# Kernel optimization log

Measured on AMD Instinct MI355X. Metric: run time of the kernel, lower is better.

Reference implementation:

```python
import jax, jax.numpy as jnp
import numpy as np

DIM = 1024
N_HEADS = 16
DIM_FF = 4096
EPS = 1e-12


def layer_norm(x, gamma, beta):
    u = jnp.mean(x, axis=-1, keepdims=True)
    s = jnp.mean((x - u) ** 2, axis=-1, keepdims=True)
    return gamma * ((x - u) / jnp.sqrt(s + EPS)) + beta


def setup_inputs() -> dict:
    key = jax.random.key(0)
    ks = jax.random.split(key, 12)
    B, S, D, F = 2, 2048, DIM, DIM_FF
    init = lambda k, shape: (jax.random.normal(k, shape, dtype=jnp.float32) * 0.02)
    return {
        "x": jax.random.normal(ks[0], (B, S, D), dtype=jnp.float32),
        "mask": jnp.ones((B, S), dtype=jnp.int32),
        "wq": init(ks[1], (D, D)), "bq": jnp.zeros((D,), jnp.float32),
        "wk": init(ks[2], (D, D)), "bk": jnp.zeros((D,), jnp.float32),
        "wv": init(ks[3], (D, D)), "bv": jnp.zeros((D,), jnp.float32),
        "wo": init(ks[4], (D, D)), "bo": jnp.zeros((D,), jnp.float32),
        "g1": jnp.ones((D,), jnp.float32), "b1": jnp.zeros((D,), jnp.float32),
        "w1": init(ks[5], (D, F)), "bf1": jnp.zeros((F,), jnp.float32),
        "w2": init(ks[6], (F, D)), "bf2": jnp.zeros((D,), jnp.float32),
        "g2": jnp.ones((D,), jnp.float32), "b2": jnp.zeros((D,), jnp.float32),
    }


def reference(x, mask, wq, bq, wk, bk, wv, bv, wo, bo, g1, b1, w1, bf1, w2, bf2, g2, b2):
    B, S, D = x.shape
    H = N_HEADS
    W = D // H
    # QKV projections -> (B, H, S, W)
    def heads(y):
        return y.reshape(B, S, H, W).transpose(0, 2, 1, 3)
    q = heads(x @ wq + bq)
    k = heads(x @ wk + bk)
    v = heads(x @ wv + bv)
    # scaled dot-product attention with additive mask (exact module math)
    scores = jnp.einsum('bhsw,bhtw->bhst', q, k) / np.sqrt(W).astype(np.float32)
    m = mask.astype(jnp.float32)[:, None, None, :]  # (B,1,1,S)
    scores = scores - 10000.0 * (1.0 - m)
    attn = jax.nn.softmax(scores, axis=-1)
    h = jnp.einsum('bhst,bhtw->bhsw', attn, v).transpose(0, 2, 1, 3).reshape(B, S, D)
    # residual + LN1
    h = layer_norm(x + (h @ wo + bo), g1, b1)
    # position-wise FFN with exact-erf GELU, residual + LN2
    ff = jax.nn.gelu(h @ w1 + bf1, approximate=False) @ w2 + bf2
    return layer_norm(h + ff, g2, b2)
```

## Files before the change

kernel.cpp:

```cpp
#include <hip/hip_runtime.h>
#include <cstdint>
#include <cstddef>

using u16 = unsigned short;
using u32 = unsigned int;

typedef __bf16 bf16x8 __attribute__((ext_vector_type(8)));
typedef float f32x4 __attribute__((ext_vector_type(4)));

static constexpr int Bb = 2, S = 2048, D = 1024, H = 16, W = 64, F = 4096;
static constexpr int M = Bb * S;

__device__ __forceinline__ float bf2f(u16 u) {
  union { u32 i; float f; } c; c.i = ((u32)u) << 16; return c.f;
}
__device__ __forceinline__ u16 f2bf(float f) {
  union { float f; u32 i; } c; c.f = f;
  u32 i = c.i;
  u32 r = (i + 0x7fffu + ((i >> 16) & 1u)) >> 16;
  return (u16)r;
}
__device__ __forceinline__ u16 f2bf_cvt(float f) {
  __bf16 b = (__bf16)f;
  union { __bf16 b; u16 u; } c; c.b = b; return c.u;
}
__device__ __forceinline__ __bf16 u2b(u16 x) {
  union { u16 u; __bf16 b; } c; c.u = x; return c.b;
}
__device__ __forceinline__ void stv(float* p, size_t i, float v) { p[i] = v; }
__device__ __forceinline__ void stv(u16* p, size_t i, float v)   { p[i] = f2bf(v); }
__device__ __forceinline__ float ldv(const float* p, size_t i) { return p[i]; }
__device__ __forceinline__ float ldv(const u16* p, size_t i)   { return bf2f(p[i]); }

__device__ __forceinline__ void async_cp16(const u16* g, u16* l) {
  __builtin_amdgcn_global_load_lds(
      (const __attribute__((address_space(1))) void*)g,
      (__attribute__((address_space(3))) void*)l, 16, 0, 0);
}

__device__ __forceinline__ void swizzle8(int& bx, int& by) {
  int bid = blockIdx.y * gridDim.x + blockIdx.x;
  int gpr = gridDim.x >> 3;
  int grp = bid >> 6, rem = bid & 63;
  int gm = grp / gpr, gn = grp - gm * gpr;
  by = gm * 8 + (rem >> 3);
  bx = gn * 8 + (rem & 7);
}

__global__ __launch_bounds__(256) void conv_x_kernel(
    const float* __restrict__ src, u16* __restrict__ dst)
{
  int i = (blockIdx.x * 256 + threadIdx.x) * 4;
  float4 v = *(const float4*)(src + i);
  u16 r[4] = { f2bf(v.x), f2bf(v.y), f2bf(v.z), f2bf(v.w) };
  *(uint2*)(dst + i) = *(const uint2*)r;
}

__global__ __launch_bounds__(256) void transpose_w_kernel(
    const float* __restrict__ src, u16* __restrict__ dst, int K, int N)
{
  __shared__ __align__(16) u16 T[64][72];
  const int tid = threadIdx.x;
  const int n0 = blockIdx.x * 64, k0 = blockIdx.y * 64;
#pragma unroll
  for (int t = 0; t < 4; t++) {
    int idx = tid + t * 256;
    int r = idx >> 4, c4 = (idx & 15) * 4;
    float4 v = *(const float4*)(src + (size_t)(k0 + r) * N + n0 + c4);
    T[c4 + 0][r] = f2bf(v.x); T[c4 + 1][r] = f2bf(v.y);
    T[c4 + 2][r] = f2bf(v.z); T[c4 + 3][r] = f2bf(v.w);
  }
  __syncthreads();
#pragma unroll
  for (int t = 0; t < 2; t++) {
    int idx = tid + t * 256;
    int r = idx >> 3, c8 = (idx & 7) * 8;
    *(uint4*)(dst + (size_t)(n0 + r) * K + k0 + c8) = *(const uint4*)(&T[r][c8]);
  }
}

template<int EPI, typename TC>
__global__ __launch_bounds__(256) void gemm_bt(
    const u16* __restrict__ A, const u16* __restrict__ BT,
    const float* __restrict__ bias, TC* __restrict__ C,
    int N, int K, float scale)
{
  __shared__ __align__(16) u16 As[2][128 * 32];
  __shared__ __align__(16) u16 Bs[2][128 * 32];
  const int tid = threadIdx.x;
  const int wave = tid >> 6, lane = tid & 63;
  const int quad = lane >> 4, l16 = lane & 15;
  int bx, by; swizzle8(bx, by);
  const int m0 = by * 128, n0 = bx * 128;
  const int wm = (wave >> 1) * 64, wn = (wave & 1) * 64;
  const int srow = lane >> 2;
  const int skoff = (lane & 3) * 8;

  f32x4 acc[4][4] = {};

  for (int k0 = 0; k0 < K; k0 += 64) {
#pragma unroll
    for (int h = 0; h < 2; h++) {
#pragma unroll
      for (int t = 0; t < 2; t++) {
        int slot = wave * 2 + t;
        int row = slot * 16 + srow;
        const u16* ga = A  + (size_t)(m0 + row) * K + k0 + h * 32 + skoff;
        const u16* gb = BT + (size_t)(n0 + row) * K + k0 + h * 32 + skoff;
        async_cp16(ga, As[h] + slot * 512);
        async_cp16(gb, Bs[h] + slot * 512);
      }
    }
    __syncthreads();

#pragma unroll
    for (int h = 0; h < 2; h++) {
      bf16x8 af[4], bfv[4];
#pragma unroll
      for (int i = 0; i < 4; i++)
        af[i] = *(const bf16x8*)(As[h] + (wm + i * 16 + l16) * 32 + quad * 8);
#pragma unroll
      for (int j = 0; j < 4; j++)
        bfv[j] = *(const bf16x8*)(Bs[h] + (wn + j * 16 + l16) * 32 + quad * 8);
#pragma unroll
      for (int i = 0; i < 4; i++)
#pragma unroll
        for (int j = 0; j < 4; j++)
          acc[i][j] = __builtin_amdgcn_mfma_f32_16x16x32_bf16(af[i], bfv[j], acc[i][j], 0, 0, 0);
    }
    __syncthreads();
  }

#pragma unroll
  for (int i = 0; i < 4; i++) {
#pragma unroll
    for (int j = 0; j < 4; j++) {
#pragma unroll
      for (int r = 0; r < 4; r++) {
        int row = m0 + wm + i * 16 + quad * 4 + r;
        int col = n0 + wn + j * 16 + l16;
        float val = acc[i][j][r] + bias[col];
        if (EPI == 1) {
          val = 0.5f * val * (1.0f + erff(val * 0.70710678118654752f));
        }
        if (EPI == 2) {
          int sel = col >> 10, c = col & 1023;
          if (sel == 0) val *= scale;
          int bb = row >> 11, ss = row & 2047;
          int hh = c >> 6,  ww = c & 63;
          u16* dst = (u16*)C + (size_t)sel * M * D;
          dst[(((size_t)(bb * H + hh) * S) + ss) * W + ww] = f2bf(val);
        } else {
          stv(C, (size_t)row * N + col, val);
        }
      }
    }
  }
}

template<typename TC>
__global__ __launch_bounds__(256) void gemm_bt_n64(
    const u16* __restrict__ A, const u16* __restrict__ BT,
    const float* __restrict__ bias, TC* __restrict__ C,
    int N, int K)
{
  __shared__ __align__(16) u16 As[2][128 * 32];
  __shared__ __align__(16) u16 Bs[2][64 * 32];
  const int tid = threadIdx.x;
  const int wave = tid >> 6, lane = tid & 63;
  const int quad = lane >> 4, l16 = lane & 15;
  int bx, by; swizzle8(bx, by);
  const int m0 = by * 128, n0 = bx * 64;
  const int wm = (wave >> 1) * 64, wn = (wave & 1) * 32;
  const int srow = lane >> 2;
  const int skoff = (lane & 3) * 8;

  f32x4 acc[4][2] = {};

  for (int k0 = 0; k0 < K; k0 += 64) {
#pragma unroll
    for (int h = 0; h < 2; h++) {
#pragma unroll
      for (int t = 0; t < 2; t++) {
        int slot = wave * 2 + t;
        int row = slot * 16 + srow;
        async_cp16(A + (size_t)(m0 + row) * K + k0 + h * 32 + skoff, As[h] + slot * 512);
      }
      int row = wave * 16 + srow;
      async_cp16(BT + (size_t)(n0 + row) * K + k0 + h * 32 + skoff, Bs[h] + wave * 512);
    }
    __syncthreads();

#pragma unroll
    for (int h = 0; h < 2; h++) {
      bf16x8 af[4], bfv[2];
#pragma unroll
      for (int i = 0; i < 4; i++)
        af[i] = *(const bf16x8*)(As[h] + (wm + i * 16 + l16) * 32 + quad * 8);
#pragma unroll
      for (int j = 0; j < 2; j++)
        bfv[j] = *(const bf16x8*)(Bs[h] + (wn + j * 16 + l16) * 32 + quad * 8);
#pragma unroll
      for (int i = 0; i < 4; i++)
#pragma unroll
        for (int j = 0; j < 2; j++)
          acc[i][j] = __builtin_amdgcn_mfma_f32_16x16x32_bf16(af[i], bfv[j], acc[i][j], 0, 0, 0);
    }
    __syncthreads();
  }

#pragma unroll
  for (int i = 0; i < 4; i++) {
#pragma unroll
    for (int j = 0; j < 2; j++) {
#pragma unroll
      for (int r = 0; r < 4; r++) {
        int row = m0 + wm + i * 16 + quad * 4 + r;
        int col = n0 + wn + j * 16 + l16;
        stv(C, (size_t)row * N + col, acc[i][j][r] + bias[col]);
      }
    }
  }
}

__global__ __launch_bounds__(256) void transpose_v_kernel(
    const u16* __restrict__ v, u16* __restrict__ vt)
{
  __shared__ __align__(16) u16 T[64][72];
  const int bh = blockIdx.y, k0 = blockIdx.x * 64, tid = threadIdx.x;
#pragma unroll
  for (int it = 0; it < 2; it++) {
    int vv = tid + it * 256;
    int key = vv >> 3, w0 = (vv & 7) * 8;
    union { uint4 q; u16 e[8]; } u;
    u.q = *(const uint4*)(v + ((size_t)bh * S + k0 + key) * W + w0);
#pragma unroll
    for (int j = 0; j < 8; j++) T[w0 + j][key] = u.e[j];
  }
  __syncthreads();
#pragma unroll
  for (int it = 0; it < 2; it++) {
    int vv = tid + it * 256;
    int w = vv >> 3, koff = (vv & 7) * 8;
    *(uint4*)(vt + ((size_t)bh * W + w) * S + k0 + koff) = *(const uint4*)(&T[w][koff]);
  }
}

__global__ __launch_bounds__(256) void fattn_kernel(
    const u16* __restrict__ q, const u16* __restrict__ k,
    const u16* __restrict__ vt, const int* __restrict__ mask,
    u16* __restrict__ o_parts, float* __restrict__ l_parts)
{
  __shared__ __align__(16) u16 QP[2][64][32];
  __shared__ __align__(16) u16 Kl[2][64][32];
  __shared__ __align__(16) u16 Vl[2][64][32];
  __shared__ float msk[64];

  const int tid = threadIdx.x, wave = tid >> 6, lane = tid & 63;
  const int quad = lane >> 4, l16 = lane & 15;
  const int bh = blockIdx.y, b = bh >> 4, h = bh & 15;
  const int q0 = blockIdx.x * 64;
  const int half = blockIdx.z;
  const int kbase = half * (S / 2);
  const int w16 = wave * 16;
  const int sr  = tid >> 3;
  const int sg  = tid & 7;
  const int sp  = sg >> 2;
  const int sc0 = sg * 8;
  const int ssw = (((sg & 3) ^ ((sr >> 1) & 3)) << 3);
  const int rq = ((quad ^ ((l16 >> 1) & 3)) << 3);

  *(uint4*)(&QP[sp][sr     ][ssw]) = *(const uint4*)(q + ((size_t)bh * S + q0 + sr     ) * W + sc0);
  *(uint4*)(&QP[sp][sr + 32][ssw]) = *(const uint4*)(q + ((size_t)bh * S + q0 + sr + 32) * W + sc0);
  __syncthreads();
  bf16x8 aq[2];
#pragma unroll
  for (int kc = 0; kc < 2; kc++)
    aq[kc] = *(const bf16x8*)(&QP[kc][w16 + l16][rq]);

  bf16x8 ones;
  {
    u16 ov = (l16 == 0) ? (u16)0x3F80 : (u16)0;
#pragma unroll
    for (int j = 0; j < 8; j++) ones[j] = u2b(ov);
  }

  f32x4 o_acc[4] = {};
  f32x4 l_acc = {};

  uint4 kr0, kr1, vr0, vr1;
  int mv = 0;
  kr0 = *(const uint4*)(k  + ((size_t)bh * S + kbase + sr     ) * W + sc0);
  kr1 = *(const uint4*)(k  + ((size_t)bh * S + kbase + sr + 32) * W + sc0);
  vr0 = *(const uint4*)(vt + ((size_t)bh * W + sr     ) * S + kbase + sc0);
  vr1 = *(const uint4*)(vt + ((size_t)bh * W + sr + 32) * S + kbase + sc0);
  if (tid < 64) mv = mask[b * S + kbase + tid];

  constexpr int NT = S / 128;
  for (int kt = 0; kt < NT; kt++) {
    __syncthreads();
    *(uint4*)(&Kl[sp][sr     ][ssw]) = kr0;
    *(uint4*)(&Kl[sp][sr + 32][ssw]) = kr1;
    *(uint4*)(&Vl[sp][sr     ][ssw]) = vr0;
    *(uint4*)(&Vl[sp][sr + 32][ssw]) = vr1;
    if (tid < 64) msk[tid] = -10000.0f * (1.0f - (float)mv);
    __syncthreads();

    if (kt + 1 < NT) {
      int kn = kbase + (kt + 1) * 64;
      kr0 = *(const uint4*)(k  + ((size_t)bh * S + kn + sr     ) * W + sc0);
      kr1 = *(const uint4*)(k  + ((size_t)bh * S + kn + sr + 32) * W + sc0);
      vr0 = *(const uint4*)(vt + ((size_t)bh * W + sr     ) * S + kn + sc0);
      vr1 = *(const uint4*)(vt + ((size_t)bh * W + sr + 32) * S + kn + sc0);
      if (tid < 64) mv = mask[b * S + kn + tid];
    }

    f32x4 sc[4] = {};
#pragma unroll
    for (int tn = 0; tn < 4; tn++) {
#pragma unroll
      for (int kc = 0; kc < 2; kc++) {
        bf16x8 bk = *(const bf16x8*)(&Kl[kc][tn * 16 + l16][rq]);
        sc[tn] = __builtin_amdgcn_mfma_f32_16x16x32_bf16(aq[kc], bk, sc[tn], 0, 0, 0);
      }
    }
#pragma unroll
    for (int tn = 0; tn < 4; tn++) {
      float mm = msk[tn * 16 + l16];
      int s0 = (tn & 1) * 2 + (l16 >> 3);
#pragma unroll
      for (int r = 0; r < 4; r++) {
        float pv = __expf(sc[tn][r] + mm);
        int xr = (quad * 2 + (r >> 1)) & 3;
        QP[tn >> 1][w16 + quad * 4 + r][((s0 ^ xr) << 3) | (l16 & 7)] = f2bf_cvt(pv);
      }
    }

#pragma unroll
    for (int kc = 0; kc < 2; kc++) {
      bf16x8 ap = *(const bf16x8*)(&QP[kc][w16 + l16][rq]);
#pragma unroll
      for (int tn = 0; tn < 4; tn++) {
        bf16x8 bv = *(const bf16x8*)(&Vl[kc][tn * 16 + l16][rq]);
        o_acc[tn] = __builtin_amdgcn_mfma_f32_16x16x32_bf16(ap, bv, o_acc[tn], 0, 0, 0);
      }
      l_acc = __builtin_amdgcn_mfma_f32_16x16x32_bf16(ap, ones, l_acc, 0, 0, 0);
    }
  }

  u16* ob = o_parts + (size_t)half * M * D;
  float* lb = l_parts + (size_t)half * M * H;
#pragma unroll
  for (int r = 0; r < 4; r++) {
    float lsum = __shfl(l_acc[r], lane & 0x30);
    int sg2 = q0 + w16 + quad * 4 + r;
    if (l16 == 0) lb[((size_t)b * S + sg2) * H + h] = lsum;
#pragma unroll
    for (int tn = 0; tn < 4; tn++) {
      ob[((size_t)b * S + sg2) * D + h * W + tn * 16 + l16] = f2bf_cvt(o_acc[tn][r]);
    }
  }
}

__global__ __launch_bounds__(256) void combine_attn(
    const u16* __restrict__ o_parts, const float* __restrict__ l_parts,
    u16* __restrict__ attn)
{
  size_t idx = ((size_t)blockIdx.x * 256 + threadIdx.x) * 8;
  int row = (int)(idx >> 10);
  int h = ((int)idx >> 6) & 15;
  float l = l_parts[(size_t)row * H + h] + l_parts[(size_t)M * H + (size_t)row * H + h];
  float inv = 1.0f / l;
  union { uint4 v; u16 e[8]; } a, bq, o;
  a.v  = *(const uint4*)(o_parts + idx);
  bq.v = *(const uint4*)(o_parts + (size_t)M * D + idx);
#pragma unroll
  for (int j = 0; j < 8; j++)
    o.e[j] = f2bf((bf2f(a.e[j]) + bf2f(bq.e[j])) * inv);
  *(uint4*)(attn + idx) = o.v;
}

template<typename TA, typename TR, typename TO>
__global__ __launch_bounds__(256) void ln_res_kernel(
    const TA* __restrict__ a, const TR* __restrict__ r,
    const float* __restrict__ g, const float* __restrict__ be,
    TO* __restrict__ out)
{
  const int tid = threadIdx.x, lane = tid & 63;
  const int row = blockIdx.x * 4 + (tid >> 6);
  const TA* ap = a + (size_t)row * D;
  const TR* rp = r + (size_t)row * D;
  float hv[16];
  float s = 0.f;
#pragma unroll
  for (int c = 0; c < 16; c++) {
    int d = c * 64 + lane;
    hv[c] = ldv(ap, d) + ldv(rp, d);
    s += hv[c];
  }
#pragma unroll
  for (int d = 1; d < 64; d <<= 1) s += __shfl_xor(s, d);
  float mean = s * (1.0f / D);
  float v = 0.f;
#pragma unroll
  for (int c = 0; c < 16; c++) { float t = hv[c] - mean; v += t * t; }
#pragma unroll
  for (int d = 1; d < 64; d <<= 1) v += __shfl_xor(v, d);
  float inv = rsqrtf(v * (1.0f / D) + 1e-12f);
#pragma unroll
  for (int c = 0; c < 16; c++) {
    int d = c * 64 + lane;
    stv(out, (size_t)row * D + d, g[d] * ((hv[c] - mean) * inv) + be[d]);
  }
}

extern "C" void kernel_launch(void* const* d_in, const int* in_sizes, int n_in,
                              void* d_out, int out_size, void* d_ws, size_t ws_size,
                              hipStream_t stream)
{
  const float* x  = (const float*)d_in[0];
  const int* mask = (const int*)d_in[1];
  const float* wq = (const float*)d_in[2];  const float* bq  = (const float*)d_in[3];
  const float* wk = (const float*)d_in[4];  const float* bk  = (const float*)d_in[5];
  const float* wv = (const float*)d_in[6];  const float* bv  = (const float*)d_in[7];
  const float* wo = (const float*)d_in[8];  const float* bo  = (const float*)d_in[9];
  const float* g1 = (const float*)d_in[10]; const float* b1  = (const float*)d_in[11];
  const float* w1 = (const float*)d_in[12]; const float* bf1 = (const float*)d_in[13];
  const float* w2 = (const float*)d_in[14]; const float* bf2 = (const float*)d_in[15];
  const float* g2 = (const float*)d_in[16]; const float* b2  = (const float*)d_in[17];

  char* ws = (char*)d_ws;
  const size_t MB = 1024 * 1024;
  u16* wqkvT = (u16*)(ws + 0 * MB);
  u16* woT   = (u16*)(ws + 6 * MB);
  u16* w1T   = (u16*)(ws + 0 * MB);
  u16* w2T   = (u16*)(ws + 0 * MB);
  u16* xb    = (u16*)(ws + 8 * MB);
  u16* vt    = (u16*)(ws + 8 * MB);
  u16* q     = (u16*)(ws + 16 * MB);
  u16* proj  = (u16*)(ws + 16 * MB);
  u16* kb    = (u16*)(ws + 24 * MB);
  u16* vb    = (u16*)(ws + 32 * MB);
  u16* oparts = (u16*)(ws + 32 * MB);
  float* lparts = (float*)(ws + 0 * MB);
  u16* attn  = (u16*)(ws + 32 * MB);
  u16* ff1   = (u16*)(ws + 8 * MB);
  float* bqkv = (float*)(ws + 40 * MB);
  u16* h1    = (u16*)(ws + 40 * MB);
  float* out = (float*)d_out;

  dim3 blk(256);

  conv_x_kernel<<<dim3(M * D / 1024), blk, 0, stream>>>(x, xb);
  transpose_w_kernel<<<dim3(16, 16), blk, 0, stream>>>(wq, wqkvT,            D, D);
  transpose_w_kernel<<<dim3(16, 16), blk, 0, stream>>>(wk, wqkvT + 1024*1024, D, D);
  transpose_w_kernel<<<dim3(16, 16), blk, 0, stream>>>(wv, wqkvT + 2048*1024, D, D);
  transpose_w_kernel<<<dim3(16, 16), blk, 0, stream>>>(wo, woT,              D, D);
  hipMemcpyAsync(bqkv,        bq, D * sizeof(float), hipMemcpyDeviceToDevice, stream);
  hipMemcpyAsync(bqkv + 1024, bk, D * sizeof(float), hipMemcpyDeviceToDevice, stream);
  hipMemcpyAsync(bqkv + 2048, bv, D * sizeof(float), hipMemcpyDeviceToDevice, stream);

  gemm_bt<2, u16><<<dim3(3072 / 128, M / 128), blk, 0, stream>>>(
      xb, wqkvT, bqkv, q, 3072, D, 0.125f);

  transpose_v_kernel<<<dim3(S / 64, Bb * H), blk, 0, stream>>>(vb, vt);
  fattn_kernel<<<dim3(S / 64, Bb * H, 2), blk, 0, stream>>>(
      q, kb, vt, mask, oparts, lparts);
  combine_attn<<<dim3(M * D / 2048), blk, 0, stream>>>(oparts, lparts, attn);

  gemm_bt_n64<u16><<<dim3(D / 64, M / 128), blk, 0, stream>>>(
      attn, woT, bo, proj, D, D);
  ln_res_kernel<float, u16, u16><<<dim3(M / 4), blk, 0, stream>>>(x, proj, g1, b1, h1);

  transpose_w_kernel<<<dim3(F / 64, D / 64), blk, 0, stream>>>(w1, w1T, D, F);
  gemm_bt<1, u16><<<dim3(F / 128, M / 128), blk, 0, stream>>>(
      h1, w1T, bf1, ff1, F, D, 1.0f);

  transpose_w_kernel<<<dim3(D / 64, F / 64), blk, 0, stream>>>(w2, w2T, F, D);
  gemm_bt_n64<float><<<dim3(D / 64, M / 128), blk, 0, stream>>>(
      ff1, w2T, bf2, out, D, F);
  ln_res_kernel<u16, float, float><<<dim3(M / 4), blk, 0, stream>>>(h1, out, g2, b2, out);
}
```

Before: 425.7 us.

## Double attention query tile per block and replace mask table with ballot bitmask

The flash-attention kernel now processes 128 query rows per block, 32 per wave, in two 16-row groups. Each K/V tile loaded into shared memory is reused across twice as many queries, and the grid is halved. The additive mask kept in shared memory is replaced by a wave ballot bitmask that multiplies the exponentials by 0 or 1. The score MFMA operands are swapped so each lane can write probabilities as packed 64-bit stores. This adds register pressure from doubled accumulators, and a fully-masked row would now produce 0/0 instead of the reference's uniform softmax.

```diff
diff --git a/kernel.cpp b/kernel.cpp
--- a/kernel.cpp
+++ b/kernel.cpp
@@ -4,6 +4,7 @@
 
 using u16 = unsigned short;
 using u32 = unsigned int;
+using u64 = unsigned long long;
 
 typedef __bf16 bf16x8 __attribute__((ext_vector_type(8)));
 typedef float f32x4 __attribute__((ext_vector_type(4)));
@@ -251,32 +252,38 @@
     const u16* __restrict__ vt, const int* __restrict__ mask,
     u16* __restrict__ o_parts, float* __restrict__ l_parts)
 {
-  __shared__ __align__(16) u16 QP[2][64][32];
+  __shared__ __align__(16) u16 QP[2][128][32];
   __shared__ __align__(16) u16 Kl[2][64][32];
   __shared__ __align__(16) u16 Vl[2][64][32];
-  __shared__ float msk[64];
 
   const int tid = threadIdx.x, wave = tid >> 6, lane = tid & 63;
   const int quad = lane >> 4, l16 = lane & 15;
   const int bh = blockIdx.y, b = bh >> 4, h = bh & 15;
-  const int q0 = blockIdx.x * 64;
+  const int q0 = blockIdx.x * 128;
   const int half = blockIdx.z;
   const int kbase = half * (S / 2);
-  const int w16 = wave * 16;
+  const int wq0 = wave * 32;
   const int sr  = tid >> 3;
   const int sg  = tid & 7;
   const int sp  = sg >> 2;
   const int sc0 = sg * 8;
   const int ssw = (((sg & 3) ^ ((sr >> 1) & 3)) << 3);
-  const int rq = ((quad ^ ((l16 >> 1) & 3)) << 3);
-
-  *(uint4*)(&QP[sp][sr     ][ssw]) = *(const uint4*)(q + ((size_t)bh * S + q0 + sr     ) * W + sc0);
-  *(uint4*)(&QP[sp][sr + 32][ssw]) = *(const uint4*)(q + ((size_t)bh * S + q0 + sr + 32) * W + sc0);
+  const int xr = (l16 >> 1) & 3;
+  const int rq = ((quad ^ xr) << 3);
+
+#pragma unroll
+  for (int t = 0; t < 4; t++) {
+    int row = sr + t * 32;
+    *(uint4*)(&QP[sp][row][ssw]) =
+        *(const uint4*)(q + ((size_t)bh * S + q0 + row) * W + sc0);
+  }
   __syncthreads();
-  bf16x8 aq[2];
-#pragma unroll
-  for (int kc = 0; kc < 2; kc++)
-    aq[kc] = *(const bf16x8*)(&QP[kc][w16 + l16][rq]);
+  bf16x8 aq[2][2];
+#pragma unroll
+  for (int g = 0; g < 2; g++)
+#pragma unroll
+    for (int kc = 0; kc < 2; kc++)
+      aq[g][kc] = *(const bf16x8*)(&QP[kc][wq0 + g * 16 + l16][rq]);
 
   bf16x8 ones;
   {
@@ -285,16 +292,16 @@
     for (int j = 0; j < 8; j++) ones[j] = u2b(ov);
   }
 
-  f32x4 o_acc[4] = {};
-  f32x4 l_acc = {};
+  f32x4 o_acc[2][4] = {};
+  f32x4 l_acc[2] = {};
 
   uint4 kr0, kr1, vr0, vr1;
-  int mv = 0;
+  int mv;
   kr0 = *(const uint4*)(k  + ((size_t)bh * S + kbase + sr     ) * W + sc0);
   kr1 = *(const uint4*)(k  + ((size_t)bh * S + kbase + sr + 32) * W + sc0);
   vr0 = *(const uint4*)(vt + ((size_t)bh * W + sr     ) * S + kbase + sc0);
   vr1 = *(const uint4*)(vt + ((size_t)bh * W + sr + 32) * S + kbase + sc0);
-  if (tid < 64) mv = mask[b * S + kbase + tid];
+  mv  = mask[b * S + kbase + lane];
 
   constexpr int NT = S / 128;
   for (int kt = 0; kt < NT; kt++) {
@@ -303,7 +310,7 @@
     *(uint4*)(&Kl[sp][sr + 32][ssw]) = kr1;
     *(uint4*)(&Vl[sp][sr     ][ssw]) = vr0;
     *(uint4*)(&Vl[sp][sr + 32][ssw]) = vr1;
-    if (tid < 64) msk[tid] = -10000.0f * (1.0f - (float)mv);
+    u64 km = __ballot(mv != 0);
     __syncthreads();
 
     if (kt + 1 < NT) {
@@ -312,52 +319,58 @@
       kr1 = *(const uint4*)(k  + ((size_t)bh * S + kn + sr + 32) * W + sc0);
       vr0 = *(const uint4*)(vt + ((size_t)bh * W + sr     ) * S + kn + sc0);
       vr1 = *(const uint4*)(vt + ((size_t)bh * W + sr + 32) * S + kn + sc0);
-      if (tid < 64) mv = mask[b * S + kn + tid];
-    }
-
-    f32x4 sc[4] = {};
+      mv  = mask[b * S + kn + lane];
+    }
+
 #pragma unroll
     for (int tn = 0; tn < 4; tn++) {
-#pragma unroll
-      for (int kc = 0; kc < 2; kc++) {
-        bf16x8 bk = *(const bf16x8*)(&Kl[kc][tn * 16 + l16][rq]);
-        sc[tn] = __builtin_amdgcn_mfma_f32_16x16x32_bf16(aq[kc], bk, sc[tn], 0, 0, 0);
-      }
-    }
-#pragma unroll
-    for (int tn = 0; tn < 4; tn++) {
-      float mm = msk[tn * 16 + l16];
-      int s0 = (tn & 1) * 2 + (l16 >> 3);
-#pragma unroll
-      for (int r = 0; r < 4; r++) {
-        float pv = __expf(sc[tn][r] + mm);
-        int xr = (quad * 2 + (r >> 1)) & 3;
-        QP[tn >> 1][w16 + quad * 4 + r][((s0 ^ xr) << 3) | (l16 & 7)] = f2bf_cvt(pv);
+      bf16x8 bk0 = *(const bf16x8*)(&Kl[0][tn * 16 + l16][rq]);
+      bf16x8 bk1 = *(const bf16x8*)(&Kl[1][tn * 16 + l16][rq]);
+      u32 nib = (u32)(km >> (tn * 16 + quad * 4)) & 0xFu;
+      int slotp = (((tn & 1) * 2 + (quad >> 1)) ^ xr) * 8 + (quad & 1) * 4;
+#pragma unroll
+      for (int g = 0; g < 2; g++) {
+        f32x4 s4 = {};
+        s4 = __builtin_amdgcn_mfma_f32_16x16x32_bf16(bk0, aq[g][0], s4, 0, 0, 0);
+        s4 = __builtin_amdgcn_mfma_f32_16x16x32_bf16(bk1, aq[g][1], s4, 0, 0, 0);
+        union { u64 u; u16 e[4]; } pw;
+#pragma unroll
+        for (int r = 0; r < 4; r++) {
+          float pm = (float)((nib >> r) & 1u);
+          pw.e[r] = f2bf_cvt(__expf(s4[r]) * pm);
+        }
+        *(u64*)(&QP[tn >> 1][wq0 + g * 16 + l16][slotp]) = pw.u;
       }
     }
 
 #pragma unroll
     for (int kc = 0; kc < 2; kc++) {
-      bf16x8 ap = *(const bf16x8*)(&QP[kc][w16 + l16][rq]);
+      bf16x8 ap0 = *(const bf16x8*)(&QP[kc][wq0      + l16][rq]);
+      bf16x8 ap1 = *(const bf16x8*)(&QP[kc][wq0 + 16 + l16][rq]);
 #pragma unroll
       for (int tn = 0; tn < 4; tn++) {
         bf16x8 bv = *(const bf16x8*)(&Vl[kc][tn * 16 + l16][rq]);
-        o_acc[tn] = __builtin_amdgcn_mfma_f32_16x16x32_bf16(ap, bv, o_acc[tn], 0, 0, 0);
-      }
-      l_acc = __builtin_amdgcn_mfma_f32_16x16x32_bf16(ap, ones, l_acc, 0, 0, 0);
+        o_acc[0][tn] = __builtin_amdgcn_mfma_f32_16x16x32_bf16(ap0, bv, o_acc[0][tn], 0, 0, 0);
+        o_acc[1][tn] = __builtin_amdgcn_mfma_f32_16x16x32_bf16(ap1, bv, o_acc[1][tn], 0, 0, 0);
+      }
+      l_acc[0] = __builtin_amdgcn_mfma_f32_16x16x32_bf16(ap0, ones, l_acc[0], 0, 0, 0);
+      l_acc[1] = __builtin_amdgcn_mfma_f32_16x16x32_bf16(ap1, ones, l_acc[1], 0, 0, 0);
     }
   }
 
   u16* ob = o_parts + (size_t)half * M * D;
   float* lb = l_parts + (size_t)half * M * H;
 #pragma unroll
-  for (int r = 0; r < 4; r++) {
-    float lsum = __shfl(l_acc[r], lane & 0x30);
-    int sg2 = q0 + w16 + quad * 4 + r;
-    if (l16 == 0) lb[((size_t)b * S + sg2) * H + h] = lsum;
-#pragma unroll
-    for (int tn = 0; tn < 4; tn++) {
-      ob[((size_t)b * S + sg2) * D + h * W + tn * 16 + l16] = f2bf_cvt(o_acc[tn][r]);
+  for (int g = 0; g < 2; g++) {
+#pragma unroll
+    for (int r = 0; r < 4; r++) {
+      float lsum = __shfl(l_acc[g][r], lane & 0x30);
+      int sg2 = q0 + wq0 + g * 16 + quad * 4 + r;
+      if (l16 == 0) lb[((size_t)b * S + sg2) * H + h] = lsum;
+#pragma unroll
+      for (int tn = 0; tn < 4; tn++) {
+        ob[((size_t)b * S + sg2) * D + h * W + tn * 16 + l16] = f2bf_cvt(o_acc[g][tn][r]);
+      }
     }
   }
 }
@@ -464,7 +477,7 @@
       xb, wqkvT, bqkv, q, 3072, D, 0.125f);
 
   transpose_v_kernel<<<dim3(S / 64, Bb * H), blk, 0, stream>>>(vb, vt);
-  fattn_kernel<<<dim3(S / 64, Bb * H, 2), blk, 0, stream>>>(
+  fattn_kernel<<<dim3(S / 128, Bb * H, 2), blk, 0, stream>>>(
       q, kb, vt, mask, oparts, lparts);
   combine_attn<<<dim3(M * D / 2048), blk, 0, stream>>>(oparts, lparts, attn);
 
```

Measured after the change: 416.4 us. 2.2% less time.
